# Kernel optimization log

Hardware: AMD Instinct MI355X
Metric: run time of the kernel (lower is better)

## Reference

```python
import jax, jax.numpy as jnp
import numpy as np

V = 50000      # vocabulary size (len(negative_sampling_table))
E = 256        # embedding_size
R = 180        # time_scope_radius -> 2R+1 = 361 time buckets
B = 2048       # batch
L = 200        # context length
NOPT = 10      # number of candidate targets (mixed_target has NOPT+1 cols)


def setup_inputs() -> dict:
    key = jax.random.key(0)
    k1, k2, k3, k4, k5, k6 = jax.random.split(key, 6)
    context = jax.random.randint(k1, (B, L, 2), 0, V, dtype=jnp.int64)
    mixed_target = jax.random.randint(k2, (B, NOPT + 1), 0, V, dtype=jnp.int64)
    context_emb_table = jax.random.normal(k3, (V, E), dtype=jnp.float32)
    target_emb_table = jax.random.normal(k4, (V, E), dtype=jnp.float32)
    taa_matrix = jax.random.uniform(k5, (V, 2 * R + 1), dtype=jnp.float32)
    taa_bias = jax.random.uniform(k6, (V, 1), dtype=jnp.float32)
    return {
        "context": context,
        "mixed_target": mixed_target,
        "context_emb_table": context_emb_table,
        "target_emb_table": target_emb_table,
        "taa_matrix": taa_matrix,
        "taa_bias": taa_bias,
    }


def reference(context, mixed_target, context_emb_table, target_emb_table, taa_matrix, taa_bias):
    radius = (taa_matrix.shape[1] - 1) // 2
    context_event = context[:, :, 0]          # [B, L]
    context_time = context[:, :, 1]           # [B, L]
    n_options = mixed_target.shape[-1] - 1
    target_event = mixed_target[:, :n_options]   # [B, n_options]
    target_time = mixed_target[:, n_options:]    # [B, 1]

    # mask padded positions (event id == -1)
    context_mask = jnp.where(context_event == -1, 0, 1)
    context_event = context_event * context_mask

    context_embedding = context_emb_table[context_event]          # [B, L, E]

    time_delta = jnp.clip(context_time - target_time + radius, 0, 2 * radius)  # [B, L]

    activated_taa = jax.nn.softmax(taa_matrix + taa_bias, axis=1)  # [V, 2R+1]
    taa_weights = activated_taa[context_event, time_delta]         # [B, L]

    # weighted masked sum over context positions
    w = taa_weights * context_mask.astype(taa_weights.dtype)       # [B, L]
    hidden = jnp.einsum("ble,bl->be", context_embedding, w)       # [B, E]

    target_embedding = target_emb_table[target_event]              # [B, n_options, E]
    scores = jnp.einsum("bne,be->bn", target_embedding, hidden)   # [B, n_options]
    return scores
```

## Files before the change

kernel.cpp:

```cpp
#include <hip/hip_runtime.h>
#include <hip/hip_bf16.h>

#define V 50000
#define E 256
#define RADIUS 180
#define TAA_W (2 * RADIUS + 1)
#define BATCH 2048
#define CTX_L 200
#define NOPT 10

__global__ __launch_bounds__(256) void taa_ise_kernel(
    const float* __restrict__ taa, float* __restrict__ inv)
{
    const int lane = threadIdx.x & 63;
    const int g    = blockIdx.x * 4 + (threadIdx.x >> 6);
    const float4* p = (const float4*)taa + (size_t)g * 361;

    float s0 = 0.f, s1 = 0.f, s2 = 0.f, s3 = 0.f;
#pragma unroll
    for (int r = 0; r < 6; ++r) {
        int j = r * 64 + lane;
        if (j < 361) {
            float4 v = p[j];
            int t = 4 * j;
            {
                float e = __expf(v.x); int u = t + 0;
                s0 += (u < 361) ? e : 0.f;
                s1 += (u >= 361 && u < 722) ? e : 0.f;
                s2 += (u >= 722 && u < 1083) ? e : 0.f;
                s3 += (u >= 1083) ? e : 0.f;
            }
            {
                float e = __expf(v.y); int u = t + 1;
                s0 += (u < 361) ? e : 0.f;
                s1 += (u >= 361 && u < 722) ? e : 0.f;
                s2 += (u >= 722 && u < 1083) ? e : 0.f;
                s3 += (u >= 1083) ? e : 0.f;
            }
            {
                float e = __expf(v.z); int u = t + 2;
                s0 += (u < 361) ? e : 0.f;
                s1 += (u >= 361 && u < 722) ? e : 0.f;
                s2 += (u >= 722 && u < 1083) ? e : 0.f;
                s3 += (u >= 1083) ? e : 0.f;
            }
            {
                float e = __expf(v.w); int u = t + 3;
                s0 += (u < 361) ? e : 0.f;
                s1 += (u >= 361 && u < 722) ? e : 0.f;
                s2 += (u >= 722 && u < 1083) ? e : 0.f;
                s3 += (u >= 1083) ? e : 0.f;
            }
        }
    }
    for (int off = 32; off > 0; off >>= 1) {
        s0 += __shfl_xor(s0, off, 64);
        s1 += __shfl_xor(s1, off, 64);
        s2 += __shfl_xor(s2, off, 64);
        s3 += __shfl_xor(s3, off, 64);
    }
    if (lane < 4) {
        float s = (lane == 0) ? s0 : (lane == 1) ? s1 : (lane == 2) ? s2 : s3;
        inv[4 * g + lane] = 1.0f / s;
    }
}

__global__ __launch_bounds__(256) void mce_taa_main_kernel(
    const int*   __restrict__ ctx,
    const int*   __restrict__ mt,
    const float* __restrict__ ctx_tab,
    const float* __restrict__ tgt_tab,
    const float* __restrict__ taa,
    const float* __restrict__ inv,
    float*       __restrict__ out)
{
    __shared__ int   s_ev[CTX_L];
    __shared__ float s_w[CTX_L];
    __shared__ float s_part[4 * E];
    __shared__ float s_hid[E];

    const int b   = blockIdx.x;
    const int tid = threadIdx.x;
    const int tgt_time = mt[b * (NOPT + 1) + NOPT];

    if (tid < CTX_L) {
        int2 ct = ((const int2*)ctx)[b * CTX_L + tid];
        int ev = ct.x, t = ct.y;
        int mask = (ev == -1) ? 0 : 1;
        ev = mask ? ev : 0;
        if (ev < 0) ev += V;
        int td = t - tgt_time + RADIUS;
        td = min(max(td, 0), 2 * RADIUS);
        float x = taa[(size_t)ev * TAA_W + td];
        float w = mask ? __expf(x) * inv[ev] : 0.f;
        s_ev[tid] = ev;
        s_w[tid]  = w;
    }
    __syncthreads();

    const int ws   = tid >> 6;
    const int lane = tid & 63;

    float a0 = 0.f, a1 = 0.f, a2 = 0.f, a3 = 0.f;
    const float4* tab4 = (const float4*)ctx_tab;
#pragma unroll 5
    for (int l0 = 0; l0 < CTX_L; l0 += 4) {
        int    l  = l0 + ws;
        int    ev = s_ev[l];
        float  w  = s_w[l];
        float4 u  = tab4[(size_t)ev * (E / 4) + lane];
        a0 = fmaf(u.x, w, a0);
        a1 = fmaf(u.y, w, a1);
        a2 = fmaf(u.z, w, a2);
        a3 = fmaf(u.w, w, a3);
    }
    {
        float* p = &s_part[ws * E + lane * 4];
        p[0] = a0; p[1] = a1; p[2] = a2; p[3] = a3;
    }
    __syncthreads();
    s_hid[tid] = s_part[tid] + s_part[E + tid] + s_part[2 * E + tid] + s_part[3 * E + tid];
    __syncthreads();

    const float4* ttab4 = (const float4*)tgt_tab;
    for (int n = ws; n < NOPT; n += 4) {
        int tg = mt[b * (NOPT + 1) + n];
        if (tg < 0) tg += V;
        float4 u = ttab4[(size_t)tg * (E / 4) + lane];
        float p = u.x * s_hid[lane * 4 + 0]
                + u.y * s_hid[lane * 4 + 1]
                + u.z * s_hid[lane * 4 + 2]
                + u.w * s_hid[lane * 4 + 3];
        for (int off = 32; off > 0; off >>= 1) p += __shfl_xor(p, off, 64);
        if (lane == 0) out[b * NOPT + n] = p;
    }
}

extern "C" void kernel_launch(void* const* d_in, const int* in_sizes, int n_in,
                              void* d_out, int out_size, void* d_ws, size_t ws_size,
                              hipStream_t stream) {
    const int*   ctx     = (const int*)d_in[0];
    const int*   mt      = (const int*)d_in[1];
    const float* ctx_tab = (const float*)d_in[2];
    const float* tgt_tab = (const float*)d_in[3];
    const float* taa     = (const float*)d_in[4];
    float* inv = (float*)d_ws;
    float* out = (float*)d_out;

    taa_ise_kernel<<<V / 16, 256, 0, stream>>>(taa, inv);
    mce_taa_main_kernel<<<BATCH, 256, 0, stream>>>(ctx, mt, ctx_tab, tgt_tab,
                                                   taa, inv, out);
}
```

Baseline: 227.8 us.

## Convert context embedding table to bf16 in prep pass and gather bf16 rows

```diff
diff --git a/kernel.cpp b/kernel.cpp
--- a/kernel.cpp
+++ b/kernel.cpp
@@ -9,66 +9,94 @@
 #define CTX_L 200
 #define NOPT 10
 
-__global__ __launch_bounds__(256) void taa_ise_kernel(
-    const float* __restrict__ taa, float* __restrict__ inv)
+#define ISE_BLOCKS  (V / 16)
+#define CONV_VEC4   (V * E / 4)
+#define CONV_BLOCKS 3125
+#define CONV_STRIDE (CONV_BLOCKS * 256)
+
+__device__ __forceinline__ unsigned short f2bf_rne(float f) {
+    unsigned u = __float_as_uint(f);
+    u += 0x7fffu + ((u >> 16) & 1u);
+    return (unsigned short)(u >> 16);
+}
+__device__ __forceinline__ unsigned pack_bf16(float a, float b) {
+    return (unsigned)f2bf_rne(a) | ((unsigned)f2bf_rne(b) << 16);
+}
+__device__ __forceinline__ float bf_lo(unsigned u) {
+    return __uint_as_float(u << 16);
+}
+__device__ __forceinline__ float bf_hi(unsigned u) {
+    return __uint_as_float(u & 0xffff0000u);
+}
+
+__global__ __launch_bounds__(256) void prep_kernel(
+    const float* __restrict__ taa, const float* __restrict__ ctx_tab,
+    float* __restrict__ inv, uint2* __restrict__ btab, int do_conv)
 {
-    const int lane = threadIdx.x & 63;
-    const int g    = blockIdx.x * 4 + (threadIdx.x >> 6);
-    const float4* p = (const float4*)taa + (size_t)g * 361;
-
-    float s0 = 0.f, s1 = 0.f, s2 = 0.f, s3 = 0.f;
+    const int blk = blockIdx.x;
+    if (blk < ISE_BLOCKS) {
+        const int lane = threadIdx.x & 63;
+        const int g    = blk * 4 + (threadIdx.x >> 6);
+        const float4* p = (const float4*)taa + (size_t)g * 361;
+        float s0 = 0.f, s1 = 0.f, s2 = 0.f, s3 = 0.f;
 #pragma unroll
-    for (int r = 0; r < 6; ++r) {
-        int j = r * 64 + lane;
-        if (j < 361) {
-            float4 v = p[j];
-            int t = 4 * j;
-            {
-                float e = __expf(v.x); int u = t + 0;
-                s0 += (u < 361) ? e : 0.f;
-                s1 += (u >= 361 && u < 722) ? e : 0.f;
-                s2 += (u >= 722 && u < 1083) ? e : 0.f;
-                s3 += (u >= 1083) ? e : 0.f;
+        for (int r = 0; r < 6; ++r) {
+            int j = r * 64 + lane;
+            if (j < 361) {
+                float4 v = p[j];
+                int t = 4 * j;
+                float e0 = __expf(v.x), e1 = __expf(v.y),
+                      e2 = __expf(v.z), e3 = __expf(v.w);
+                int u0 = t, u1 = t + 1, u2 = t + 2, u3 = t + 3;
+                s0 += (u0 < 361) ? e0 : 0.f;
+                s1 += (u0 >= 361 && u0 < 722) ? e0 : 0.f;
+                s2 += (u0 >= 722 && u0 < 1083) ? e0 : 0.f;
+                s3 += (u0 >= 1083) ? e0 : 0.f;
+                s0 += (u1 < 361) ? e1 : 0.f;
+                s1 += (u1 >= 361 && u1 < 722) ? e1 : 0.f;
+                s2 += (u1 >= 722 && u1 < 1083) ? e1 : 0.f;
+                s3 += (u1 >= 1083) ? e1 : 0.f;
+                s0 += (u2 < 361) ? e2 : 0.f;
+                s1 += (u2 >= 361 && u2 < 722) ? e2 : 0.f;
+                s2 += (u2 >= 722 && u2 < 1083) ? e2 : 0.f;
+                s3 += (u2 >= 1083) ? e2 : 0.f;
+                s0 += (u3 < 361) ? e3 : 0.f;
+                s1 += (u3 >= 361 && u3 < 722) ? e3 : 0.f;
+                s2 += (u3 >= 722 && u3 < 1083) ? e3 : 0.f;
+                s3 += (u3 >= 1083) ? e3 : 0.f;
             }
-            {
-                float e = __expf(v.y); int u = t + 1;
-                s0 += (u < 361) ? e : 0.f;
-                s1 += (u >= 361 && u < 722) ? e : 0.f;
-                s2 += (u >= 722 && u < 1083) ? e : 0.f;
-                s3 += (u >= 1083) ? e : 0.f;
-            }
-            {
-                float e = __expf(v.z); int u = t + 2;
-                s0 += (u < 361) ? e : 0.f;
-                s1 += (u >= 361 && u < 722) ? e : 0.f;
-                s2 += (u >= 722 && u < 1083) ? e : 0.f;
-                s3 += (u >= 1083) ? e : 0.f;
-            }
-            {
-                float e = __expf(v.w); int u = t + 3;
-                s0 += (u < 361) ? e : 0.f;
-                s1 += (u >= 361 && u < 722) ? e : 0.f;
-                s2 += (u >= 722 && u < 1083) ? e : 0.f;
-                s3 += (u >= 1083) ? e : 0.f;
-            }
-        }
-    }
-    for (int off = 32; off > 0; off >>= 1) {
-        s0 += __shfl_xor(s0, off, 64);
-        s1 += __shfl_xor(s1, off, 64);
-        s2 += __shfl_xor(s2, off, 64);
-        s3 += __shfl_xor(s3, off, 64);
-    }
-    if (lane < 4) {
-        float s = (lane == 0) ? s0 : (lane == 1) ? s1 : (lane == 2) ? s2 : s3;
-        inv[4 * g + lane] = 1.0f / s;
-    }
-}
-
+        }
+        for (int off = 32; off > 0; off >>= 1) {
+            s0 += __shfl_xor(s0, off, 64);
+            s1 += __shfl_xor(s1, off, 64);
+            s2 += __shfl_xor(s2, off, 64);
+            s3 += __shfl_xor(s3, off, 64);
+        }
+        if (lane < 4) {
+            float s = (lane == 0) ? s0 : (lane == 1) ? s1 : (lane == 2) ? s2 : s3;
+            inv[4 * g + lane] = 1.0f / s;
+        }
+    } else if (do_conv) {
+        const float4* src = (const float4*)ctx_tab;
+        size_t base = (size_t)(blk - ISE_BLOCKS) * 256 + threadIdx.x;
+#pragma unroll
+        for (int r = 0; r < 4; ++r) {
+            size_t i = base + (size_t)r * CONV_STRIDE;
+            float4 v = src[i];
+            uint2 o;
+            o.x = pack_bf16(v.x, v.y);
+            o.y = pack_bf16(v.z, v.w);
+            btab[i] = o;
+        }
+    }
+}
+
+template <int USE_BF16>
 __global__ __launch_bounds__(256) void mce_taa_main_kernel(
     const int*   __restrict__ ctx,
     const int*   __restrict__ mt,
     const float* __restrict__ ctx_tab,
+    const uint2* __restrict__ btab,
     const float* __restrict__ tgt_tab,
     const float* __restrict__ taa,
     const float* __restrict__ inv,
@@ -92,9 +120,8 @@
         int td = t - tgt_time + RADIUS;
         td = min(max(td, 0), 2 * RADIUS);
         float x = taa[(size_t)ev * TAA_W + td];
-        float w = mask ? __expf(x) * inv[ev] : 0.f;
         s_ev[tid] = ev;
-        s_w[tid]  = w;
+        s_w[tid]  = mask ? __expf(x) * inv[ev] : 0.f;
     }
     __syncthreads();
 
@@ -102,17 +129,31 @@
     const int lane = tid & 63;
 
     float a0 = 0.f, a1 = 0.f, a2 = 0.f, a3 = 0.f;
-    const float4* tab4 = (const float4*)ctx_tab;
-#pragma unroll 5
-    for (int l0 = 0; l0 < CTX_L; l0 += 4) {
-        int    l  = l0 + ws;
-        int    ev = s_ev[l];
-        float  w  = s_w[l];
-        float4 u  = tab4[(size_t)ev * (E / 4) + lane];
-        a0 = fmaf(u.x, w, a0);
-        a1 = fmaf(u.y, w, a1);
-        a2 = fmaf(u.z, w, a2);
-        a3 = fmaf(u.w, w, a3);
+    if (USE_BF16) {
+#pragma unroll 10
+        for (int l0 = 0; l0 < CTX_L; l0 += 4) {
+            int   l  = l0 + ws;
+            int   ev = s_ev[l];
+            float w  = s_w[l];
+            uint2 u  = btab[(size_t)ev * (E / 4) + lane];
+            a0 = fmaf(bf_lo(u.x), w, a0);
+            a1 = fmaf(bf_hi(u.x), w, a1);
+            a2 = fmaf(bf_lo(u.y), w, a2);
+            a3 = fmaf(bf_hi(u.y), w, a3);
+        }
+    } else {
+        const float4* tab4 = (const float4*)ctx_tab;
+#pragma unroll 10
+        for (int l0 = 0; l0 < CTX_L; l0 += 4) {
+            int    l  = l0 + ws;
+            int    ev = s_ev[l];
+            float  w  = s_w[l];
+            float4 u  = tab4[(size_t)ev * (E / 4) + lane];
+            a0 = fmaf(u.x, w, a0);
+            a1 = fmaf(u.y, w, a1);
+            a2 = fmaf(u.z, w, a2);
+            a3 = fmaf(u.w, w, a3);
+        }
     }
     {
         float* p = &s_part[ws * E + lane * 4];
@@ -144,10 +185,20 @@
     const float* ctx_tab = (const float*)d_in[2];
     const float* tgt_tab = (const float*)d_in[3];
     const float* taa     = (const float*)d_in[4];
-    float* inv = (float*)d_ws;
     float* out = (float*)d_out;
 
-    taa_ise_kernel<<<V / 16, 256, 0, stream>>>(taa, inv);
-    mce_taa_main_kernel<<<BATCH, 256, 0, stream>>>(ctx, mt, ctx_tab, tgt_tab,
-                                                   taa, inv, out);
-}
+    float* inv  = (float*)d_ws;
+    uint2* btab = (uint2*)((char*)d_ws + (256 << 10));
+    const size_t need = (256 << 10) + (size_t)V * E * 2;
+    const int use_bf16 = (ws_size >= need) ? 1 : 0;
+
+    prep_kernel<<<ISE_BLOCKS + (use_bf16 ? CONV_BLOCKS : 0), 256, 0, stream>>>(
+        taa, ctx_tab, inv, btab, use_bf16);
+    if (use_bf16) {
+        mce_taa_main_kernel<1><<<BATCH, 256, 0, stream>>>(
+            ctx, mt, ctx_tab, btab, tgt_tab, taa, inv, out);
+    } else {
+        mce_taa_main_kernel<0><<<BATCH, 256, 0, stream>>>(
+            ctx, mt, ctx_tab, btab, tgt_tab, taa, inv, out);
+    }
+}
```

Result: faster. 215.3 us (-5.5%).
